# Kernel tuning notes

Hardware: AMD Instinct MI355X
Metric: run time of the kernel (lower is better)

The kernel has to match this reference:

```python
import jax, jax.numpy as jnp
import numpy as np


def setup_inputs() -> dict:
    key = jax.random.key(0)
    ks = jax.random.split(key, 8)
    B, IN, H, OUT = 8192, 1024, 2048, 1024
    SIGMA_MIN, SIGMA_MAX, PHASE = 0.9, 0.999, 2.0 * np.pi
    # recurrence decay params, initialized as in the torch module
    rng = np.random.RandomState(0)
    u1 = rng.random_sample(H)
    u2 = rng.random_sample(H)
    v = -0.5 * np.log(u1 * (SIGMA_MAX ** 2 - SIGMA_MIN ** 2) + SIGMA_MIN ** 2)
    theta = u2 * PHASE
    scale_b = 1.0 / np.sqrt(IN)
    scale_c = 1.0 / np.sqrt(H)
    return {
        "x": jax.random.normal(ks[0], (B, IN), dtype=jnp.float32),
        "h_prev": jax.random.normal(ks[1], (B, H), dtype=jnp.float32),
        "Br": jax.random.normal(ks[2], (H, IN), dtype=jnp.float32) * scale_b,
        "Bi": jax.random.normal(ks[3], (H, IN), dtype=jnp.float32) * scale_b,
        "Cr": jax.random.normal(ks[4], (OUT, H), dtype=jnp.float32) * scale_c,
        "Ci": jax.random.normal(ks[5], (OUT, H), dtype=jnp.float32) * scale_c,
        "v_log": jnp.asarray(np.log(v), dtype=jnp.float32),
        "theta_log": jnp.asarray(np.log(theta), dtype=jnp.float32),
    }


def reference(x, h_prev, Br, Bi, Cr, Ci, v_log, theta_log):
    # effective diagonal recurrence weight w = exp(-exp(v_log) + i*exp(theta_log))
    mag = jnp.exp(-jnp.exp(v_log))            # [H]
    ang = jnp.exp(theta_log)                  # [H]
    wr = mag * jnp.cos(ang)
    wi = mag * jnp.sin(ang)
    # h = B(x) + h_prev * w  (h_prev is real -> imag part comes only from wi)
    # complexLinear on real x: real = x@Br^T, imag = x@Bi^T
    hr = jnp.einsum('bi,hi->bh', x, Br) + h_prev * wr   # [B,H]
    hi = jnp.einsum('bi,hi->bh', x, Bi) + h_prev * wi   # [B,H]
    # out = Re(C(h)) = hr@Cr^T - hi@Ci^T
    out = jnp.einsum('bh,oh->bo', hr, Cr) - jnp.einsum('bh,oh->bo', hi, Ci)
    return out
```

## Files before the change

### kernel.cpp

```cpp
#include <hip/hip_runtime.h>
#include <stdint.h>

typedef unsigned short u16;
typedef short bf16x8 __attribute__((ext_vector_type(8)));
typedef float f32x4 __attribute__((ext_vector_type(4)));

typedef void as1_void __attribute__((address_space(1)));
typedef void as3_void __attribute__((address_space(3)));

__device__ inline u16 f32_to_bf16(float f) {
    uint32_t u = __builtin_bit_cast(uint32_t, f);
    u += 0x7fffu + ((u >> 16) & 1u);
    return (u16)(u >> 16);
}

__device__ inline void gld_lds16(const void* g, void* l) {
    __builtin_amdgcn_global_load_lds((as1_void*)g, (as3_void*)l, 16, 0, 0);
}



__global__ void prep_w_kernel(const float* __restrict__ v_log,
                              const float* __restrict__ theta_log,
                              float* __restrict__ wfull, int H) {
    int h = blockIdx.x * blockDim.x + threadIdx.x;
    if (h < H) {
        float mag = expf(-expf(v_log[h]));
        float ang = expf(theta_log[h]);
        wfull[h]     = mag * cosf(ang);
        wfull[h + H] = mag * sinf(ang);
    }
}

__global__ void pack_ccat_kernel(const float* __restrict__ Cr,
                                 const float* __restrict__ Ci,
                                 u16* __restrict__ Ccat, int total4) {
    int i = blockIdx.x * blockDim.x + threadIdx.x;
    if (i >= total4) return;
    int e = i * 4;
    int o = e >> 12;
    int k = e & 4095;
    float4 f; float s;
    if (k < 2048) { f = *(const float4*)(Cr + (size_t)o * 2048 + k);          s =  1.f; }
    else          { f = *(const float4*)(Ci + (size_t)o * 2048 + (k - 2048)); s = -1.f; }
    ushort4 u;
    u.x = f32_to_bf16(s * f.x); u.y = f32_to_bf16(s * f.y);
    u.z = f32_to_bf16(s * f.z); u.w = f32_to_bf16(s * f.w);
    ((ushort4*)Ccat)[i] = u;
}

__global__ void transpose_cast_kernel(const float* __restrict__ Br,
                                      const float* __restrict__ Bi,
                                      u16* __restrict__ Bcat) {
    __shared__ float t[32][33];
    const float* src = blockIdx.z ? Bi : Br;
    int colOff = blockIdx.z ? 2048 : 0;
    int c0 = blockIdx.x * 32, r0 = blockIdx.y * 32;
    int tx = threadIdx.x, ty = threadIdx.y;
#pragma unroll
    for (int j = 0; j < 4; j++)
        t[ty + j * 8][tx] = src[(size_t)(r0 + ty + j * 8) * 1024 + c0 + tx];
    __syncthreads();
#pragma unroll
    for (int j = 0; j < 4; j++)
        Bcat[(size_t)(c0 + ty + j * 8) * 4096 + colOff + r0 + tx] =
            f32_to_bf16(t[tx][ty + j * 8]);
}

__global__ void cast_both_kernel(const float* __restrict__ x,
                                 const float* __restrict__ h_prev,
                                 u16* __restrict__ dst) {
    const int n4x = 8192 * 1024 / 4;
    int i = blockIdx.x * blockDim.x + threadIdx.x;
    float4 f = (i < n4x) ? ((const float4*)x)[i] : ((const float4*)h_prev)[i - n4x];
    ushort4 o;
    o.x = f32_to_bf16(f.x); o.y = f32_to_bf16(f.y);
    o.z = f32_to_bf16(f.z); o.w = f32_to_bf16(f.w);
    ((ushort4*)dst)[i] = o;
}

__global__ void reduce_cw_kernel(const float* __restrict__ partials,
                                 const float* __restrict__ Cr, const float* __restrict__ Ci,
                                 const float* __restrict__ wfull,
                                 u16* __restrict__ Wmain, u16* __restrict__ Cwbf) {
    const int n4_red = 1024 * 1024 / 4;
    const int n4_cw  = 1024 * 2048 / 4;
    int i = blockIdx.x * blockDim.x + threadIdx.x;
    if (i < n4_red) {
        int e = i * 4;
        float4 s = *(const float4*)(partials + e);
#pragma unroll
        for (int z = 1; z < 8; z++) {
            float4 p = *(const float4*)(partials + ((size_t)z << 20) + e);
            s.x += p.x; s.y += p.y; s.z += p.z; s.w += p.w;
        }
        ushort4 u;
        u.x = f32_to_bf16(s.x); u.y = f32_to_bf16(s.y);
        u.z = f32_to_bf16(s.z); u.w = f32_to_bf16(s.w);
        ((ushort4*)Wmain)[i] = u;
    } else if (i < n4_red + n4_cw) {
        int j = i - n4_red;
        int e = j * 4;
        int o = e >> 11;
        int h = e & 2047;
        float4 cr = *(const float4*)(Cr + (size_t)o * 2048 + h);
        float4 ci = *(const float4*)(Ci + (size_t)o * 2048 + h);
        float4 wr = *(const float4*)(wfull + h);
        float4 wi = *(const float4*)(wfull + 2048 + h);
        ushort4 u;
        u.x = f32_to_bf16(cr.x * wr.x - ci.x * wi.x);
        u.y = f32_to_bf16(cr.y * wr.y - ci.y * wi.y);
        u.z = f32_to_bf16(cr.z * wr.z - ci.z * wi.z);
        u.w = f32_to_bf16(cr.w * wr.w - ci.w * wi.w);
        ((ushort4*)Cwbf)[j] = u;
    }
}


__global__ __launch_bounds__(256)
void gemm_splitk_kernel(const u16* __restrict__ A, const u16* __restrict__ B,
                        float* __restrict__ partials)
{
    __shared__ __align__(16) u16 ldsA[128 * 64];
    __shared__ __align__(16) u16 ldsB[128 * 64];
    const int K = 4096;

    const int tid = threadIdx.x, wid = tid >> 6, lane = tid & 63;
    const int quad = lane >> 4, l16 = lane & 15;
    const int wm = wid >> 1, wn = wid & 1;
    const int bm = blockIdx.y, bn = blockIdx.x, bz = blockIdx.z;
    const int kb = bz * 512;

    const u16* gA[4]; const u16* gB[4];
    u16 *lA[4], *lB[4];
#pragma unroll
    for (int t = 0; t < 4; t++) {
        int s = wid * 256 + t * 64 + lane;
        int sr = s >> 3;
        int sj = (s & 7) ^ (sr & 7);
        lA[t] = ldsA + s * 8;
        lB[t] = ldsB + s * 8;
        gA[t] = A + (size_t)(bm * 128 + sr) * K + sj * 8 + kb;
        gB[t] = B + (size_t)(bn * 128 + sr) * K + sj * 8 + kb;
    }

    const f32x4 fz = {0.f, 0.f, 0.f, 0.f};
    f32x4 acc[4][4];
#pragma unroll
    for (int i = 0; i < 4; i++)
#pragma unroll
        for (int j = 0; j < 4; j++) acc[i][j] = fz;

    for (int k0 = 0; k0 < 512; k0 += 64) {
        __syncthreads();
#pragma unroll
        for (int t = 0; t < 4; t++) {
            gld_lds16(gA[t] + k0, lA[t]);
            gld_lds16(gB[t] + k0, lB[t]);
        }
        __syncthreads();
#pragma unroll
        for (int ks = 0; ks < 2; ks++) {
            bf16x8 af[4], bfr[4];
#pragma unroll
            for (int i = 0; i < 4; i++) {
                int r = wm * 64 + i * 16 + l16;
                af[i] = *(const bf16x8*)(ldsA + (r * 8 + ((ks * 4 + quad) ^ (r & 7))) * 8);
            }
#pragma unroll
            for (int j = 0; j < 4; j++) {
                int r = wn * 64 + j * 16 + l16;
                bfr[j] = *(const bf16x8*)(ldsB + (r * 8 + ((ks * 4 + quad) ^ (r & 7))) * 8);
            }
#pragma unroll
            for (int i = 0; i < 4; i++)
#pragma unroll
                for (int j = 0; j < 4; j++)
                    acc[i][j] = __builtin_amdgcn_mfma_f32_16x16x32_bf16(af[i], bfr[j], acc[i][j], 0, 0, 0);
        }
    }

    float* P = partials + ((size_t)bz << 20);
    const int gm = bm * 128 + wm * 64, gn = bn * 128 + wn * 64;
#pragma unroll
    for (int i = 0; i < 4; i++)
#pragma unroll
        for (int j = 0; j < 4; j++) {
            int col = gn + j * 16 + l16;
#pragma unroll
            for (int r = 0; r < 4; r++)
                P[(size_t)(gm + i * 16 + quad * 4 + r) * 1024 + col] = acc[i][j][r];
        }
}


__global__ __launch_bounds__(256)
void gemm_main_kernel(const u16* __restrict__ Axb, const u16* __restrict__ Ahb,
                      const u16* __restrict__ Bw,  const u16* __restrict__ Bcw,
                      float* __restrict__ out)
{
    __shared__ __align__(16) u16 ldsA[128 * 64];
    __shared__ __align__(16) u16 ldsB[128 * 64];

    const int tid = threadIdx.x, wid = tid >> 6, lane = tid & 63;
    const int quad = lane >> 4, l16 = lane & 15;
    const int wm = wid >> 1, wn = wid & 1;
    const int id = blockIdx.x;
    const int bm = id & 63, bn = id >> 6;

    int srow[4], sj[4];
    u16 *lA[4], *lB[4];
#pragma unroll
    for (int t = 0; t < 4; t++) {
        int s = wid * 256 + t * 64 + lane;
        srow[t] = s >> 3;
        sj[t] = (s & 7) ^ (srow[t] & 7);
        lA[t] = ldsA + s * 8;
        lB[t] = ldsB + s * 8;
    }

    const f32x4 fz = {0.f, 0.f, 0.f, 0.f};
    f32x4 acc[4][4];
#pragma unroll
    for (int i = 0; i < 4; i++)
#pragma unroll
        for (int j = 0; j < 4; j++) acc[i][j] = fz;

#pragma unroll 1
    for (int phase = 0; phase < 2; phase++) {
        const u16* Ap = phase ? Ahb : Axb;
        const u16* Bp = phase ? Bcw : Bw;
        const int KS = phase ? 2048 : 1024;
        const u16* gA[4]; const u16* gB[4];
#pragma unroll
        for (int t = 0; t < 4; t++) {
            gA[t] = Ap + (size_t)(bm * 128 + srow[t]) * KS + sj[t] * 8;
            gB[t] = Bp + (size_t)(bn * 128 + srow[t]) * KS + sj[t] * 8;
        }
        for (int k0 = 0; k0 < KS; k0 += 64) {
            __syncthreads();
#pragma unroll
            for (int t = 0; t < 4; t++) {
                gld_lds16(gA[t] + k0, lA[t]);
                gld_lds16(gB[t] + k0, lB[t]);
            }
            __syncthreads();
#pragma unroll
            for (int ks = 0; ks < 2; ks++) {
                bf16x8 af[4], bfr[4];
#pragma unroll
                for (int i = 0; i < 4; i++) {
                    int r = wm * 64 + i * 16 + l16;
                    af[i] = *(const bf16x8*)(ldsA + (r * 8 + ((ks * 4 + quad) ^ (r & 7))) * 8);
                }
#pragma unroll
                for (int j = 0; j < 4; j++) {
                    int r = wn * 64 + j * 16 + l16;
                    bfr[j] = *(const bf16x8*)(ldsB + (r * 8 + ((ks * 4 + quad) ^ (r & 7))) * 8);
                }
#pragma unroll
                for (int i = 0; i < 4; i++)
#pragma unroll
                    for (int j = 0; j < 4; j++)
                        acc[i][j] = __builtin_amdgcn_mfma_f32_16x16x32_bf16(af[i], bfr[j], acc[i][j], 0, 0, 0);
            }
        }
    }

    const int gm = bm * 128 + wm * 64, gn = bn * 128 + wn * 64;
#pragma unroll
    for (int i = 0; i < 4; i++)
#pragma unroll
        for (int j = 0; j < 4; j++) {
            int col = gn + j * 16 + l16;
#pragma unroll
            for (int r = 0; r < 4; r++)
                out[(size_t)(gm + i * 16 + quad * 4 + r) * 1024 + col] = acc[i][j][r];
        }
}


extern "C" void kernel_launch(void* const* d_in, const int* in_sizes, int n_in,
                              void* d_out, int out_size, void* d_ws, size_t ws_size,
                              hipStream_t stream)
{
    const float* x      = (const float*)d_in[0];
    const float* h_prev = (const float*)d_in[1];
    const float* Br     = (const float*)d_in[2];
    const float* Bi     = (const float*)d_in[3];
    const float* Cr     = (const float*)d_in[4];
    const float* Ci     = (const float*)d_in[5];
    const float* v_log  = (const float*)d_in[6];
    const float* th_log = (const float*)d_in[7];
    float* out = (float*)d_out;

    const size_t MB = 1024 * 1024;
    size_t need = 54 * MB + 4096 * 4;
    if (ws_size < need) return;

    char* ws = (char*)d_ws;
    u16*   Ccat     = (u16*)ws;
    u16*   Bcat     = (u16*)(ws + 8 * MB);
    float* partials = (float*)(ws + 16 * MB);
    u16*   x_bf     = (u16*)ws;
    u16*   hp_bf    = (u16*)(ws + 16 * MB);
    u16*   Wmain    = (u16*)(ws + 48 * MB);
    u16*   Cwbf     = (u16*)(ws + 50 * MB);
    float* wfull    = (float*)(ws + 54 * MB);

    prep_w_kernel<<<8, 256, 0, stream>>>(v_log, th_log, wfull, 2048);
    pack_ccat_kernel<<<4096, 256, 0, stream>>>(Cr, Ci, Ccat, 1024 * 4096 / 4);
    transpose_cast_kernel<<<dim3(32, 64, 2), dim3(32, 8), 0, stream>>>(Br, Bi, Bcat);
    gemm_splitk_kernel<<<dim3(8, 8, 8), 256, 0, stream>>>(Ccat, Bcat, partials);
    reduce_cw_kernel<<<3072, 256, 0, stream>>>(partials, Cr, Ci, wfull, Wmain, Cwbf);
    cast_both_kernel<<<24576, 256, 0, stream>>>(x, h_prev, x_bf);
    gemm_main_kernel<<<512, 256, 0, stream>>>(x_bf, hp_bf, Wmain, Cwbf, out);
}
```

Before: 251.4 us.

## Merge prep kernels and fuse split-K reduction into last-arriving GEMM block

Three prep kernels (w computation, C packing, B transpose) and the Cw computation are merged into one launch, with w recomputed inline per element instead of staged through a workspace buffer. The split-K weight GEMM now uses an atomic counter per output tile so that the last-arriving block sums the eight partial slices and writes the bf16 Wmain, replacing the separate reduce kernel. This cuts the number of kernel launches and removes one pass over the partials. In exchange it adds a threadfence/atomic handshake, a serial reduction in a single block per tile, and redundant transcendental work per element.

```diff
diff --git a/kernel.cpp b/kernel.cpp
--- a/kernel.cpp
+++ b/kernel.cpp
@@ -20,51 +20,63 @@
 
 
 
-__global__ void prep_w_kernel(const float* __restrict__ v_log,
-                              const float* __restrict__ theta_log,
-                              float* __restrict__ wfull, int H) {
-    int h = blockIdx.x * blockDim.x + threadIdx.x;
-    if (h < H) {
-        float mag = expf(-expf(v_log[h]));
-        float ang = expf(theta_log[h]);
-        wfull[h]     = mag * cosf(ang);
-        wfull[h + H] = mag * sinf(ang);
-    }
-}
-
-__global__ void pack_ccat_kernel(const float* __restrict__ Cr,
-                                 const float* __restrict__ Ci,
-                                 u16* __restrict__ Ccat, int total4) {
-    int i = blockIdx.x * blockDim.x + threadIdx.x;
-    if (i >= total4) return;
-    int e = i * 4;
-    int o = e >> 12;
-    int k = e & 4095;
-    float4 f; float s;
-    if (k < 2048) { f = *(const float4*)(Cr + (size_t)o * 2048 + k);          s =  1.f; }
-    else          { f = *(const float4*)(Ci + (size_t)o * 2048 + (k - 2048)); s = -1.f; }
-    ushort4 u;
-    u.x = f32_to_bf16(s * f.x); u.y = f32_to_bf16(s * f.y);
-    u.z = f32_to_bf16(s * f.z); u.w = f32_to_bf16(s * f.w);
-    ((ushort4*)Ccat)[i] = u;
-}
-
-__global__ void transpose_cast_kernel(const float* __restrict__ Br,
-                                      const float* __restrict__ Bi,
-                                      u16* __restrict__ Bcat) {
+__global__ void prep_kernel(const float* __restrict__ Cr, const float* __restrict__ Ci,
+                            const float* __restrict__ Br, const float* __restrict__ Bi,
+                            const float* __restrict__ v_log, const float* __restrict__ th_log,
+                            u16* __restrict__ Ccat, u16* __restrict__ Bcat,
+                            u16* __restrict__ Cwbf, int* __restrict__ cnt)
+{
     __shared__ float t[32][33];
-    const float* src = blockIdx.z ? Bi : Br;
-    int colOff = blockIdx.z ? 2048 : 0;
-    int c0 = blockIdx.x * 32, r0 = blockIdx.y * 32;
-    int tx = threadIdx.x, ty = threadIdx.y;
-#pragma unroll
-    for (int j = 0; j < 4; j++)
-        t[ty + j * 8][tx] = src[(size_t)(r0 + ty + j * 8) * 1024 + c0 + tx];
-    __syncthreads();
-#pragma unroll
-    for (int j = 0; j < 4; j++)
-        Bcat[(size_t)(c0 + ty + j * 8) * 4096 + colOff + r0 + tx] =
-            f32_to_bf16(t[tx][ty + j * 8]);
+    const int b = blockIdx.x, tid = threadIdx.x;
+    if (b == 0 && tid < 64) cnt[tid] = 0;
+
+    if (b < 4096) {
+        int i = b * 256 + tid;
+        int e = i * 4;
+        int o = e >> 12;
+        int k = e & 4095;
+        float4 f; float s;
+        if (k < 2048) { f = *(const float4*)(Cr + (size_t)o * 2048 + k);          s =  1.f; }
+        else          { f = *(const float4*)(Ci + (size_t)o * 2048 + (k - 2048)); s = -1.f; }
+        ushort4 u;
+        u.x = f32_to_bf16(s * f.x); u.y = f32_to_bf16(s * f.y);
+        u.z = f32_to_bf16(s * f.z); u.w = f32_to_bf16(s * f.w);
+        ((ushort4*)Ccat)[i] = u;
+    } else if (b < 8192) {
+        int b2 = b - 4096;
+        const float* src = (b2 & 2048) ? Bi : Br;
+        int colOff = (b2 & 2048) ? 2048 : 0;
+        int c0 = (b2 & 31) * 32, r0 = ((b2 >> 5) & 63) * 32;
+        int tx = tid & 31, ty = tid >> 5;
+#pragma unroll
+        for (int j = 0; j < 4; j++)
+            t[ty + j * 8][tx] = src[(size_t)(r0 + ty + j * 8) * 1024 + c0 + tx];
+        __syncthreads();
+#pragma unroll
+        for (int j = 0; j < 4; j++)
+            Bcat[(size_t)(c0 + ty + j * 8) * 4096 + colOff + r0 + tx] =
+                f32_to_bf16(t[tx][ty + j * 8]);
+    } else {
+        int j = (b - 8192) * 256 + tid;
+        int e = j * 4;
+        int o = e >> 11;
+        int h = e & 2047;
+        float4 cr = *(const float4*)(Cr + (size_t)o * 2048 + h);
+        float4 ci = *(const float4*)(Ci + (size_t)o * 2048 + h);
+        float4 vl = *(const float4*)(v_log + h);
+        float4 tl = *(const float4*)(th_log + h);
+        float mag, ang, wr, wi;
+        ushort4 u;
+        mag = expf(-expf(vl.x)); ang = expf(tl.x); wr = mag * cosf(ang); wi = mag * sinf(ang);
+        u.x = f32_to_bf16(cr.x * wr - ci.x * wi);
+        mag = expf(-expf(vl.y)); ang = expf(tl.y); wr = mag * cosf(ang); wi = mag * sinf(ang);
+        u.y = f32_to_bf16(cr.y * wr - ci.y * wi);
+        mag = expf(-expf(vl.z)); ang = expf(tl.z); wr = mag * cosf(ang); wi = mag * sinf(ang);
+        u.z = f32_to_bf16(cr.z * wr - ci.z * wi);
+        mag = expf(-expf(vl.w)); ang = expf(tl.w); wr = mag * cosf(ang); wi = mag * sinf(ang);
+        u.w = f32_to_bf16(cr.w * wr - ci.w * wi);
+        ((ushort4*)Cwbf)[j] = u;
+    }
 }
 
 __global__ void cast_both_kernel(const float* __restrict__ x,
@@ -79,50 +91,15 @@
     ((ushort4*)dst)[i] = o;
 }
 
-__global__ void reduce_cw_kernel(const float* __restrict__ partials,
-                                 const float* __restrict__ Cr, const float* __restrict__ Ci,
-                                 const float* __restrict__ wfull,
-                                 u16* __restrict__ Wmain, u16* __restrict__ Cwbf) {
-    const int n4_red = 1024 * 1024 / 4;
-    const int n4_cw  = 1024 * 2048 / 4;
-    int i = blockIdx.x * blockDim.x + threadIdx.x;
-    if (i < n4_red) {
-        int e = i * 4;
-        float4 s = *(const float4*)(partials + e);
-#pragma unroll
-        for (int z = 1; z < 8; z++) {
-            float4 p = *(const float4*)(partials + ((size_t)z << 20) + e);
-            s.x += p.x; s.y += p.y; s.z += p.z; s.w += p.w;
-        }
-        ushort4 u;
-        u.x = f32_to_bf16(s.x); u.y = f32_to_bf16(s.y);
-        u.z = f32_to_bf16(s.z); u.w = f32_to_bf16(s.w);
-        ((ushort4*)Wmain)[i] = u;
-    } else if (i < n4_red + n4_cw) {
-        int j = i - n4_red;
-        int e = j * 4;
-        int o = e >> 11;
-        int h = e & 2047;
-        float4 cr = *(const float4*)(Cr + (size_t)o * 2048 + h);
-        float4 ci = *(const float4*)(Ci + (size_t)o * 2048 + h);
-        float4 wr = *(const float4*)(wfull + h);
-        float4 wi = *(const float4*)(wfull + 2048 + h);
-        ushort4 u;
-        u.x = f32_to_bf16(cr.x * wr.x - ci.x * wi.x);
-        u.y = f32_to_bf16(cr.y * wr.y - ci.y * wi.y);
-        u.z = f32_to_bf16(cr.z * wr.z - ci.z * wi.z);
-        u.w = f32_to_bf16(cr.w * wr.w - ci.w * wi.w);
-        ((ushort4*)Cwbf)[j] = u;
-    }
-}
-
 
 __global__ __launch_bounds__(256)
 void gemm_splitk_kernel(const u16* __restrict__ A, const u16* __restrict__ B,
-                        float* __restrict__ partials)
+                        float* __restrict__ partials, u16* __restrict__ Wmain,
+                        int* __restrict__ cnt)
 {
     __shared__ __align__(16) u16 ldsA[128 * 64];
     __shared__ __align__(16) u16 ldsB[128 * 64];
+    __shared__ int lastFlag;
     const int K = 4096;
 
     const int tid = threadIdx.x, wid = tid >> 6, lane = tid & 63;
@@ -190,6 +167,30 @@
 #pragma unroll
             for (int r = 0; r < 4; r++)
                 P[(size_t)(gm + i * 16 + quad * 4 + r) * 1024 + col] = acc[i][j][r];
+        }
+
+    __threadfence();
+    __syncthreads();
+    if (tid == 0)
+        lastFlag = (atomicAdd(&cnt[bm * 8 + bn], 1) == 7);
+    __syncthreads();
+    if (!lastFlag) return;
+    __threadfence();
+
+#pragma unroll
+    for (int i = 0; i < 4; i++)
+#pragma unroll
+        for (int j = 0; j < 4; j++) {
+            int col = gn + j * 16 + l16;
+#pragma unroll
+            for (int r = 0; r < 4; r++) {
+                size_t off = (size_t)(gm + i * 16 + quad * 4 + r) * 1024 + col;
+                float s = 0.f;
+#pragma unroll
+                for (int z = 0; z < 8; z++)
+                    s += partials[((size_t)z << 20) + off];
+                Wmain[off] = f32_to_bf16(s);
+            }
         }
 }
 
@@ -295,7 +296,7 @@
     float* out = (float*)d_out;
 
     const size_t MB = 1024 * 1024;
-    size_t need = 54 * MB + 4096 * 4;
+    size_t need = 54 * MB + 256;
     if (ws_size < need) return;
 
     char* ws = (char*)d_ws;
@@ -306,13 +307,11 @@
     u16*   hp_bf    = (u16*)(ws + 16 * MB);
     u16*   Wmain    = (u16*)(ws + 48 * MB);
     u16*   Cwbf     = (u16*)(ws + 50 * MB);
-    float* wfull    = (float*)(ws + 54 * MB);
-
-    prep_w_kernel<<<8, 256, 0, stream>>>(v_log, th_log, wfull, 2048);
-    pack_ccat_kernel<<<4096, 256, 0, stream>>>(Cr, Ci, Ccat, 1024 * 4096 / 4);
-    transpose_cast_kernel<<<dim3(32, 64, 2), dim3(32, 8), 0, stream>>>(Br, Bi, Bcat);
-    gemm_splitk_kernel<<<dim3(8, 8, 8), 256, 0, stream>>>(Ccat, Bcat, partials);
-    reduce_cw_kernel<<<3072, 256, 0, stream>>>(partials, Cr, Ci, wfull, Wmain, Cwbf);
+    int*   cnt      = (int*)(ws + 54 * MB);
+
+    prep_kernel<<<10240, 256, 0, stream>>>(Cr, Ci, Br, Bi, v_log, th_log,
+                                           Ccat, Bcat, Cwbf, cnt);
+    gemm_splitk_kernel<<<dim3(8, 8, 8), 256, 0, stream>>>(Ccat, Bcat, partials, Wmain, cnt);
     cast_both_kernel<<<24576, 256, 0, stream>>>(x, h_prev, x_bf);
     gemm_main_kernel<<<512, 256, 0, stream>>>(x_bf, hp_bf, Wmain, Cwbf, out);
 }
```

Result: slower. 322.0 us (+28.0%).
